# Performance work log

Hardware: AMD Instinct MI355X
Metric: run time of the kernel (lower is better)

The kernel has to match this reference:

```python
import jax, jax.numpy as jnp
import numpy as np

N = 65536        # gaussians
NTILE = 8        # tiles per side
TS = 64          # tile size in pixels
T = NTILE * NTILE
K = 256          # depth-sorted gaussians per tile
W = H = NTILE * TS


def setup_inputs() -> dict:
    key = jax.random.key(0)
    ks = jax.random.split(key, 6)
    mu = jax.random.uniform(ks[0], (N, 2), dtype=jnp.float32) * W   # 2D screen means
    L = jax.random.normal(ks[1], (N, 2, 2), dtype=jnp.float32) * 2.0
    # PSD 2x2 covariances with a few-pixel footprint
    cov2d = jnp.einsum('nij,nkj->nik', L, L) + 4.0 * jnp.eye(2, dtype=jnp.float32)
    opacity = jax.random.uniform(ks[2], (N,), dtype=jnp.float32)
    color = jax.random.uniform(ks[3], (N, 3), dtype=jnp.float32)
    depth = jax.random.uniform(ks[4], (N,), dtype=jnp.float32)
    idx = jax.random.randint(ks[5], (T, K), 0, N)
    # depth-sort gaussians within each tile (Screen.depth_sort)
    order = jnp.argsort(depth[idx], axis=1)
    tile_idx = jnp.take_along_axis(idx, order, axis=1).astype(jnp.int32)
    return {"mu": mu, "cov2d": cov2d, "opacity": opacity, "color": color,
            "tile_idx": tile_idx}


def _rasterize(mu, cov2d, opacity, color, tile_idx):
    # closed-form 2x2 inverse of cov2d
    a = cov2d[:, 0, 0]; b = cov2d[:, 0, 1]
    c = cov2d[:, 1, 0]; d = cov2d[:, 1, 1]
    det = jnp.maximum(a * d - b * c, 1e-6)
    inv = jnp.stack([jnp.stack([d, -b], -1),
                     jnp.stack([-c, a], -1)], -2) / det[:, None, None]  # [N,2,2]

    ly, lx = jnp.meshgrid(jnp.arange(TS), jnp.arange(TS), indexing='ij')
    local = (jnp.stack([lx, ly], -1).reshape(TS * TS, 2).astype(jnp.float32)
             + 0.5)  # pixel centers within a tile, [P,2]

    def tile_fn(args):
        tid, idx = args
        ty = tid // NTILE
        tx = tid % NTILE
        origin = jnp.stack([tx * TS, ty * TS]).astype(jnp.float32)
        pix = local + origin                              # [P,2]
        m = mu[idx]                                       # [K,2]
        ic = inv[idx]                                     # [K,2,2]
        op = opacity[idx]                                 # [K]
        col = color[idx]                                  # [K,3]
        dlt = pix[:, None, :] - m[None, :, :]             # [P,K,2]
        maha = jnp.einsum('pki,kij,pkj->pk', dlt, ic, dlt)
        prob = jnp.exp(-0.5 * maha)                       # [P,K]
        alpha = jnp.clip(op[None, :] * prob, 0.01, 0.99)
        # weight_i = alpha_i * (1 - sum_{j<i} alpha_j)  (shifted cumsum, as in source)
        trans = 1.0 - (jnp.cumsum(alpha, axis=1) - alpha)
        w = alpha * trans                                 # [P,K]
        return (w @ col).reshape(TS, TS, 3)

    tiles = jax.lax.map(tile_fn, (jnp.arange(T, dtype=jnp.int32), tile_idx))  # [T,TS,TS,3]
    img = tiles.reshape(NTILE, NTILE, TS, TS, 3)
    img = img.transpose(0, 2, 1, 3, 4).reshape(H, W, 3)
    return img


def reference(mu, cov2d, opacity, color, tile_idx):
    return _rasterize(mu, cov2d, opacity, color, tile_idx)
```

## Files before the change

kernel.cpp:

```cpp
#include <hip/hip_runtime.h>
#include <math.h>

#define TS 64
#define T 64
#define K 256
#define NSEG 4
#define KSEG 64
#define IMG_W 512

__global__ __launch_bounds__(512, 4) void render_all(
    const float* __restrict__ mu, const float* __restrict__ cov,
    const float* __restrict__ opacity, const float* __restrict__ color,
    const int* __restrict__ tile_idx, float* __restrict__ out) {
  __shared__ float4 sA[K];
  __shared__ float4 sB[K];
  __shared__ float sC[K];
  __shared__ float sR[K];
  __shared__ float4 sbuf[2 * K];
  __shared__ float4 sPA[K + 1];
  __shared__ float4 sPK[K + 1];
  __shared__ float sS[NSEG][128][4];
  __shared__ float sD[3][128][4][3];

  int tid = threadIdx.x;
  int blk = blockIdx.x;
  int tile = blk & 63;
  int chunk = blk >> 6;

  if (tid < K) {
    int n = tile_idx[tile * K + tid];
    float a = cov[4 * n + 0];
    float b = cov[4 * n + 1];
    float c = cov[4 * n + 2];
    float d = cov[4 * n + 3];
    float det = fmaxf(a * d - b * c, 1e-6f);
    const float LOG2E = 1.4426950408889634f;
    float s = -0.5f * LOG2E / det;
    float mx = mu[2 * n], my = mu[2 * n + 1];
    float lop = log2f(fmaxf(opacity[n], 1e-30f));
    float cr = color[3 * n], cg = color[3 * n + 1], cb = color[3 * n + 2];
    sA[tid] = make_float4(mx, my, s * d, -s * (b + c));
    sB[tid] = make_float4(s * a, lop, cr, cg);
    sC[tid] = cb;
    float r2 = 1.3862943611f * (lop + 6.6438561898f) * (a + d);
    sR[tid] = r2 * 1.0001f + 1e-3f;
    sbuf[tid] = make_float4(cr, cg, cb, 0.f);
    float fk = (float)tid;
    sbuf[K + tid] = make_float4(fk * cr, fk * cg, fk * cb, 0.f);
  }
  __syncthreads();

  int lane256 = tid & 255;
  float4* mybuf = sbuf + (tid & 256);
  for (int off = 1; off < K; off <<= 1) {
    float4 t;
    bool act = lane256 >= off;
    if (act) t = mybuf[lane256 - off];
    __syncthreads();
    if (act) {
      float4 u = mybuf[lane256];
      mybuf[lane256] = make_float4(u.x + t.x, u.y + t.y, u.z + t.z, 0.f);
    }
    __syncthreads();
  }
  if (tid < K) {
    sPA[tid + 1] = sbuf[tid];
  } else {
    sPK[lane256 + 1] = sbuf[K + lane256];
  }
  if (tid == 0) {
    sPA[0] = make_float4(0.f, 0.f, 0.f, 0.f);
    sPK[0] = make_float4(0.f, 0.f, 0.f, 0.f);
  }
  __syncthreads();

  int seg = __builtin_amdgcn_readfirstlane(tid >> 7);
  int pslot = tid & 127;
  int lx = pslot & 63;
  int bnd = __builtin_amdgcn_readfirstlane(chunk * 2 + ((tid >> 6) & 1));
  int ty = tile >> 3, tx = tile & 7;
  int ly0 = bnd * 4;
  float px = (float)(tx * TS + lx) + 0.5f;
  float py0 = (float)(ty * TS + ly0) + 0.5f;
  const int kb = seg * KSEG;

  unsigned long long m;
  {
    int l = tid & 63;
    float4 Ag = sA[kb + l];
    float r2 = sR[kb + l];
    float x0 = tx * TS + 0.5f, x1 = tx * TS + 63.5f;
    float y0 = py0, y1 = py0 + 3.0f;
    float dxm = fmaxf(fmaxf(Ag.x - x1, x0 - Ag.x), 0.f);
    float dym = fmaxf(fmaxf(Ag.y - y1, y0 - Ag.y), 0.f);
    float d2 = fmaf(dxm, dxm, dym * dym);
    m = __ballot(d2 < r2);
  }

  float C[4][3] = {};
  float An[4][3] = {};
  float Af[3] = {0.f, 0.f, 0.f};
  float S[4] = {};

  int i = kb;
  while (true) {
    int j = (m != 0ULL) ? (kb + (int)__builtin_ctzll(m)) : (kb + KSEG);
    if (j > i) {
      float len = (float)(j - i);
      float4 paj = sPA[j], pai = sPA[i];
      float4 pkj = sPK[j], pki = sPK[i];
      float P1r = paj.x - pai.x, P1g = paj.y - pai.y, P1b = paj.z - pai.z;
      float fi = (float)i;
      float Rr = -1e-4f * fmaf(-fi, P1r, pkj.x - pki.x);
      float Rg = -1e-4f * fmaf(-fi, P1g, pkj.y - pki.y);
      float Rb = -1e-4f * fmaf(-fi, P1b, pkj.z - pki.z);
      Af[0] = fmaf(0.01f, P1r, Af[0]);
      Af[1] = fmaf(0.01f, P1g, Af[1]);
      Af[2] = fmaf(0.01f, P1b, Af[2]);
#pragma unroll
      for (int p = 0; p < 4; ++p) {
        float t = fmaf(-0.01f, S[p], 0.01f);
        C[p][0] = fmaf(t, P1r, C[p][0]) + Rr;
        C[p][1] = fmaf(t, P1g, C[p][1]) + Rg;
        C[p][2] = fmaf(t, P1b, C[p][2]) + Rb;
        S[p] = fmaf(0.01f, len, S[p]);
      }
    }
    if (j >= kb + KSEG) break;
    float4 A4 = sA[j];
    float4 B4 = sB[j];
    float cbv = sC[j];
    float dx = px - A4.x;
    float tb = A4.w * dx;
    float base = fmaf(A4.z * dx, dx, B4.y);
    float dy = py0 - A4.y;
#pragma unroll
    for (int p = 0; p < 4; ++p) {
      float dyp = dy + (float)p;
      float mm = fmaf(dyp, fmaf(B4.x, dyp, tb), base);
      float al =
          __builtin_amdgcn_fmed3f(__builtin_amdgcn_exp2f(mm), 0.01f, 0.99f);
      float w = fmaf(-al, S[p], al);
      C[p][0] = fmaf(w, B4.z, C[p][0]);
      C[p][1] = fmaf(w, B4.w, C[p][1]);
      C[p][2] = fmaf(w, cbv, C[p][2]);
      An[p][0] = fmaf(al, B4.z, An[p][0]);
      An[p][1] = fmaf(al, B4.w, An[p][1]);
      An[p][2] = fmaf(al, cbv, An[p][2]);
      S[p] += al;
    }
    m &= (m - 1ULL);
    i = j + 1;
  }

#pragma unroll
  for (int p = 0; p < 4; ++p) sS[seg][pslot][p] = S[p];
  __syncthreads();

  if (seg >= 1) {
#pragma unroll
    for (int p = 0; p < 4; ++p) {
      float Sp = sS[0][pslot][p];
      if (seg >= 2) Sp += sS[1][pslot][p];
      if (seg >= 3) Sp += sS[2][pslot][p];
      sD[seg - 1][pslot][p][0] = fmaf(-Sp, An[p][0] + Af[0], C[p][0]);
      sD[seg - 1][pslot][p][1] = fmaf(-Sp, An[p][1] + Af[1], C[p][1]);
      sD[seg - 1][pslot][p][2] = fmaf(-Sp, An[p][2] + Af[2], C[p][2]);
    }
  }
  __syncthreads();

  if (seg == 0) {
    int x = tx * TS + lx;
#pragma unroll
    for (int p = 0; p < 4; ++p) {
      int y = ty * TS + ly0 + p;
      size_t o = ((size_t)y * IMG_W + x) * 3;
      out[o + 0] = C[p][0] + sD[0][pslot][p][0] + sD[1][pslot][p][0] +
                   sD[2][pslot][p][0];
      out[o + 1] = C[p][1] + sD[0][pslot][p][1] + sD[1][pslot][p][1] +
                   sD[2][pslot][p][1];
      out[o + 2] = C[p][2] + sD[0][pslot][p][2] + sD[1][pslot][p][2] +
                   sD[2][pslot][p][2];
    }
  }
}

extern "C" void kernel_launch(void* const* d_in, const int* in_sizes, int n_in,
                              void* d_out, int out_size, void* d_ws,
                              size_t ws_size, hipStream_t stream) {
  const float* mu = (const float*)d_in[0];
  const float* cov = (const float*)d_in[1];
  const float* opacity = (const float*)d_in[2];
  const float* color = (const float*)d_in[3];
  const int* tile_idx = (const int*)d_in[4];
  float* out = (float*)d_out;
  (void)d_ws;
  (void)ws_size;

  render_all<<<T * 8, 512, 0, stream>>>(mu, cov, opacity, color, tile_idx,
                                        out);
}
```

Before: 69.19 us.

## Split per-tile gaussian staging and prefix scans into a separate pre-pass kernel

Gaussian parameter setup and the per-tile colour prefix sums move out of the render kernel into a staging kernel with one block per tile. That kernel computes the scans with wavefront shuffles and writes packed float4 records to workspace. Before, each of the 8 render blocks per tile repeated the gather and an 8-step barrier-heavy shared-memory scan. The render kernel now only loads precomputed records into shared memory, at the cost of an extra kernel launch and a global round trip through the workspace.

New measurement: 69.25 us. About the same (+0.1%).

```diff
diff --git a/kernel.cpp b/kernel.cpp
--- a/kernel.cpp
+++ b/kernel.cpp
@@ -8,15 +8,89 @@
 #define KSEG 64
 #define IMG_W 512
 
-__global__ __launch_bounds__(512, 4) void render_all(
+
+__global__ __launch_bounds__(256, 4) void stage_tiles(
     const float* __restrict__ mu, const float* __restrict__ cov,
     const float* __restrict__ opacity, const float* __restrict__ color,
-    const int* __restrict__ tile_idx, float* __restrict__ out) {
+    const int* __restrict__ tile_idx, float4* __restrict__ ws) {
+  __shared__ float wtot[4][8];
+
+  int k = threadIdx.x;
+  int tile = blockIdx.x;
+  int lane = k & 63;
+  int w = k >> 6;
+
+  int n = tile_idx[tile * K + k];
+  float a = cov[4 * n + 0];
+  float b = cov[4 * n + 1];
+  float c = cov[4 * n + 2];
+  float d = cov[4 * n + 3];
+  float det = fmaxf(a * d - b * c, 1e-6f);
+  const float LOG2E = 1.4426950408889634f;
+  float s = -0.5f * LOG2E / det;
+  float mx = mu[2 * n], my = mu[2 * n + 1];
+  float lop = log2f(fmaxf(opacity[n], 1e-30f));
+  float cr = color[3 * n], cg = color[3 * n + 1], cb = color[3 * n + 2];
+  float r2 = 1.3862943611f * (lop + 6.6438561898f) * (a + d);
+  r2 = r2 * 1.0001f + 1e-3f;
+
+  float fk = (float)k;
+  float v0 = cr, v1 = cg, v2 = cb;
+  float v3 = fk * cr, v4 = fk * cg, v5 = fk * cb;
+
+#pragma unroll
+  for (int off = 1; off < 64; off <<= 1) {
+    float t0 = __shfl_up(v0, off, 64);
+    float t1 = __shfl_up(v1, off, 64);
+    float t2 = __shfl_up(v2, off, 64);
+    float t3 = __shfl_up(v3, off, 64);
+    float t4 = __shfl_up(v4, off, 64);
+    float t5 = __shfl_up(v5, off, 64);
+    if (lane >= off) {
+      v0 += t0;
+      v1 += t1;
+      v2 += t2;
+      v3 += t3;
+      v4 += t4;
+      v5 += t5;
+    }
+  }
+  if (lane == 63) {
+    wtot[w][0] = v0;
+    wtot[w][1] = v1;
+    wtot[w][2] = v2;
+    wtot[w][3] = v3;
+    wtot[w][4] = v4;
+    wtot[w][5] = v5;
+  }
+  __syncthreads();
+  float o0 = 0.f, o1 = 0.f, o2 = 0.f, o3 = 0.f, o4 = 0.f, o5 = 0.f;
+  for (int ww = 0; ww < w; ++ww) {
+    o0 += wtot[ww][0];
+    o1 += wtot[ww][1];
+    o2 += wtot[ww][2];
+    o3 += wtot[ww][3];
+    o4 += wtot[ww][4];
+    o5 += wtot[ww][5];
+  }
+  v0 += o0;
+  v1 += o1;
+  v2 += o2;
+  v3 += o3;
+  v4 += o4;
+  v5 += o5;
+
+  int base = tile * K + k;
+  ws[0 * T * K + base] = make_float4(mx, my, s * d, -s * (b + c));
+  ws[1 * T * K + base] = make_float4(s * a, lop, cr, cg);
+  ws[2 * T * K + base] = make_float4(v0, v1, v2, cb);
+  ws[3 * T * K + base] = make_float4(v3, v4, v5, r2);
+}
+
+__global__ __launch_bounds__(512, 4) void render_all(
+    const float4* __restrict__ ws, float* __restrict__ out) {
   __shared__ float4 sA[K];
   __shared__ float4 sB[K];
-  __shared__ float sC[K];
-  __shared__ float sR[K];
-  __shared__ float4 sbuf[2 * K];
   __shared__ float4 sPA[K + 1];
   __shared__ float4 sPK[K + 1];
   __shared__ float sS[NSEG][128][4];
@@ -27,50 +101,22 @@
   int tile = blk & 63;
   int chunk = blk >> 6;
 
-  if (tid < K) {
-    int n = tile_idx[tile * K + tid];
-    float a = cov[4 * n + 0];
-    float b = cov[4 * n + 1];
-    float c = cov[4 * n + 2];
-    float d = cov[4 * n + 3];
-    float det = fmaxf(a * d - b * c, 1e-6f);
-    const float LOG2E = 1.4426950408889634f;
-    float s = -0.5f * LOG2E / det;
-    float mx = mu[2 * n], my = mu[2 * n + 1];
-    float lop = log2f(fmaxf(opacity[n], 1e-30f));
-    float cr = color[3 * n], cg = color[3 * n + 1], cb = color[3 * n + 2];
-    sA[tid] = make_float4(mx, my, s * d, -s * (b + c));
-    sB[tid] = make_float4(s * a, lop, cr, cg);
-    sC[tid] = cb;
-    float r2 = 1.3862943611f * (lop + 6.6438561898f) * (a + d);
-    sR[tid] = r2 * 1.0001f + 1e-3f;
-    sbuf[tid] = make_float4(cr, cg, cb, 0.f);
-    float fk = (float)tid;
-    sbuf[K + tid] = make_float4(fk * cr, fk * cg, fk * cb, 0.f);
-  }
-  __syncthreads();
-
-  int lane256 = tid & 255;
-  float4* mybuf = sbuf + (tid & 256);
-  for (int off = 1; off < K; off <<= 1) {
-    float4 t;
-    bool act = lane256 >= off;
-    if (act) t = mybuf[lane256 - off];
-    __syncthreads();
-    if (act) {
-      float4 u = mybuf[lane256];
-      mybuf[lane256] = make_float4(u.x + t.x, u.y + t.y, u.z + t.z, 0.f);
-    }
-    __syncthreads();
-  }
-  if (tid < K) {
-    sPA[tid + 1] = sbuf[tid];
-  } else {
-    sPK[lane256 + 1] = sbuf[K + lane256];
-  }
-  if (tid == 0) {
-    sPA[0] = make_float4(0.f, 0.f, 0.f, 0.f);
-    sPK[0] = make_float4(0.f, 0.f, 0.f, 0.f);
+  {
+    int q = tid >> 8;
+    int k = tid & 255;
+    float4 r0 = ws[q * T * K + tile * K + k];
+    float4 r1 = ws[(q + 2) * T * K + tile * K + k];
+    if (q == 0) {
+      sA[k] = r0;
+      sPA[k + 1] = r1;
+    } else {
+      sB[k] = r0;
+      sPK[k + 1] = r1;
+    }
+    if (tid == 0) {
+      sPA[0] = make_float4(0.f, 0.f, 0.f, 0.f);
+      sPK[0] = make_float4(0.f, 0.f, 0.f, 0.f);
+    }
   }
   __syncthreads();
 
@@ -88,7 +134,7 @@
   {
     int l = tid & 63;
     float4 Ag = sA[kb + l];
-    float r2 = sR[kb + l];
+    float r2 = sPK[kb + l + 1].w;
     float x0 = tx * TS + 0.5f, x1 = tx * TS + 63.5f;
     float y0 = py0, y1 = py0 + 3.0f;
     float dxm = fmaxf(fmaxf(Ag.x - x1, x0 - Ag.x), 0.f);
@@ -129,7 +175,7 @@
     if (j >= kb + KSEG) break;
     float4 A4 = sA[j];
     float4 B4 = sB[j];
-    float cbv = sC[j];
+    float cbv = sPA[j + 1].w;
     float dx = px - A4.x;
     float tb = A4.w * dx;
     float base = fmaf(A4.z * dx, dx, B4.y);
@@ -195,9 +241,12 @@
   const float* color = (const float*)d_in[3];
   const int* tile_idx = (const int*)d_in[4];
   float* out = (float*)d_out;
-  (void)d_ws;
+  float4* ws = (float4*)d_ws;
+  (void)in_sizes;
+  (void)n_in;
+  (void)out_size;
   (void)ws_size;
 
-  render_all<<<T * 8, 512, 0, stream>>>(mu, cov, opacity, color, tile_idx,
-                                        out);
+  stage_tiles<<<T, 256, 0, stream>>>(mu, cov, opacity, color, tile_idx, ws);
+  render_all<<<T * 8, 512, 0, stream>>>(ws, out);
 }
```
